# Kernel optimization log

Hardware: AMD Instinct MI355X
Metric: run time of the kernel (lower is better)

The kernel has to match this reference:

```python
import jax, jax.numpy as jnp
import numpy as np

NUM_HEADS = 12


def setup_inputs() -> dict:
    key = jax.random.key(0)
    k1, k2, k3 = jax.random.split(key, 3)
    B, N, C = 64, 320, 768
    x = jax.random.normal(k1, (B, N, C), dtype=jnp.float32)
    W_qkv = jax.random.normal(k2, (C, 3 * C), dtype=jnp.float32) * (C ** -0.5)
    W_proj = jax.random.normal(k3, (C, C), dtype=jnp.float32) * (C ** -0.5)
    b_proj = jnp.zeros((C,), dtype=jnp.float32)
    return {"x": x, "W_qkv": W_qkv, "W_proj": W_proj, "b_proj": b_proj,
            "t_h": 8, "t_w": 8, "s_h": 16, "s_w": 16}


def reference(x, W_qkv, W_proj, b_proj, t_h, t_w, s_h, s_w):
    B, N, C = x.shape
    H = NUM_HEADS
    Dh = C // H
    scale = Dh ** -0.5
    L = t_h * t_w  # template length; search length = s_h*s_w = N - L

    qkv = (x @ W_qkv).reshape(B, N, 3, H, Dh)
    q = jnp.transpose(qkv[:, :, 0], (0, 2, 1, 3))  # [B,H,N,Dh]
    k = jnp.transpose(qkv[:, :, 1], (0, 2, 1, 3))
    v = jnp.transpose(qkv[:, :, 2], (0, 2, 1, 3))

    q_mt, q_s = q[:, :, :L], q[:, :, L:]
    k_mt = k[:, :, :L]
    v_mt = v[:, :, :L]

    # Template self-attention (template attends only to template)
    attn_mt = jax.nn.softmax(jnp.einsum('bhqd,bhkd->bhqk', q_mt * scale, k_mt), axis=-1)
    x_mt = jnp.einsum('bhqk,bhkd->bhqd', attn_mt, v_mt)  # [B,H,L,Dh]

    # Search cross-attention (search attends to all tokens)
    attn_s = jax.nn.softmax(jnp.einsum('bhqd,bhkd->bhqk', q_s * scale, k), axis=-1)
    x_s = jnp.einsum('bhqk,bhkd->bhqd', attn_s, v)  # [B,H,N-L,Dh]

    x_mt = jnp.transpose(x_mt, (0, 2, 1, 3)).reshape(B, L, C)
    x_s = jnp.transpose(x_s, (0, 2, 1, 3)).reshape(B, N - L, C)
    out = jnp.concatenate([x_mt, x_s], axis=1)  # [B,N,C]
    out = out @ W_proj + b_proj
    return out
```

## Files before the change

kernel.cpp:

```cpp
#include <hip/hip_runtime.h>
#include <hip/hip_bf16.h>
#include <stdint.h>

#define BB 64
#define NN 320
#define CC 768
#define HH 12
#define DH 64
#define NC3 2304
#define MROWS (BB*NN)

typedef __attribute__((ext_vector_type(8))) short short8;
typedef __attribute__((ext_vector_type(4))) float f32x4;
typedef __attribute__((ext_vector_type(8))) __bf16 bf16x8;

union BF8U { short8 s; bf16x8 b; };
static __device__ __forceinline__ bf16x8 asbf(short8 v){ BF8U u; u.s = v; return u.b; }

#define MFMA16(a,b,c) __builtin_amdgcn_mfma_f32_16x16x32_bf16((a),(b),(c),0,0,0)

static __device__ __forceinline__ void gload16(const void* g, void* l){
  __builtin_amdgcn_global_load_lds(
      (const __attribute__((address_space(1))) void*)g,
      (__attribute__((address_space(3))) void*)l, 16, 0, 0);
}

__global__ __launch_bounds__(256) void convert_wT(
    const float* __restrict__ in, __hip_bfloat16* __restrict__ outT,
    int K, int Nc)
{
  __shared__ __hip_bfloat16 t[64][72];
  const int n0 = blockIdx.x * 64, k0 = blockIdx.y * 64;
  const int tid = threadIdx.x;
  const int tx = tid & 15, ty = tid >> 4;

  #pragma unroll
  for (int i = 0; i < 4; ++i){
    int kl = ty + i * 16;
    float4 v = *reinterpret_cast<const float4*>(&in[(size_t)(k0 + kl) * Nc + n0 + tx * 4]);
    t[tx*4+0][kl] = __float2bfloat16(v.x);
    t[tx*4+1][kl] = __float2bfloat16(v.y);
    t[tx*4+2][kl] = __float2bfloat16(v.z);
    t[tx*4+3][kl] = __float2bfloat16(v.w);
  }
  __syncthreads();
  #pragma unroll
  for (int j = 0; j < 2; ++j){
    int nl = (tid >> 3) + j * 32;
    int kl = (tid & 7) * 8;
    short8 v = *reinterpret_cast<const short8*>(&t[nl][kl]);
    *reinterpret_cast<short8*>(&outT[(size_t)(n0 + nl) * K + k0 + kl]) = v;
  }
}

__global__ __launch_bounds__(256) void convert_x(
    const float* __restrict__ X, __hip_bfloat16* __restrict__ Xb)
{
  size_t i = ((size_t)blockIdx.x * 256 + threadIdx.x) * 8;
  float4 a = *reinterpret_cast<const float4*>(&X[i]);
  float4 b = *reinterpret_cast<const float4*>(&X[i + 4]);
  __hip_bfloat16 t[8] = {__float2bfloat16(a.x), __float2bfloat16(a.y),
                         __float2bfloat16(a.z), __float2bfloat16(a.w),
                         __float2bfloat16(b.x), __float2bfloat16(b.y),
                         __float2bfloat16(b.z), __float2bfloat16(b.w)};
  *reinterpret_cast<short8*>(&Xb[i]) = *reinterpret_cast<const short8*>(t);
}

#define BM 128
#define BN 128
#define BK 64
#define NT (CC/BK)

__global__ __launch_bounds__(256, 4) void gemm_qkv(
    const __hip_bfloat16* __restrict__ Xb,
    const __hip_bfloat16* __restrict__ WT,
    __hip_bfloat16* __restrict__ qb,
    __hip_bfloat16* __restrict__ kb,
    __hip_bfloat16* __restrict__ vt)
{
  __shared__ __hip_bfloat16 As[BM][BK];
  __shared__ __hip_bfloat16 Bs[BN][BK];
  const int tid = threadIdx.x;
  const int bm = blockIdx.x * BM;
  const int bn = blockIdx.y * BN;
  const int w = tid >> 6, lane = tid & 63;
  const int wr = w >> 1, wc = w & 1;
  const int l16 = lane & 15, lq = lane >> 4;
  const int srow = lane >> 3;
  const int scol = ((lane & 7) ^ srow) * 8;
  const int rsw  = (l16 & 7) * 8;

  f32x4 acc[4][4];
  #pragma unroll
  for (int i = 0; i < 4; ++i)
    #pragma unroll
    for (int j = 0; j < 4; ++j) acc[i][j] = (f32x4){0.f,0.f,0.f,0.f};

  for (int k0 = 0; k0 < CC; k0 += BK){
    #pragma unroll
    for (int it = 0; it < 4; ++it){
      int c = w * 4 + it;
      int row = c * 8 + srow;
      gload16(&Xb[(size_t)(bm + row) * CC + k0 + scol], &As[0][0] + c * 512);
      gload16(&WT[(size_t)(bn + row) * CC + k0 + scol], &Bs[0][0] + c * 512);
    }
    __syncthreads();
    #pragma unroll
    for (int kc = 0; kc < 2; ++kc){
      const int acol = (kc*32 + lq*8) ^ rsw;
      short8 bfr[4];
      #pragma unroll
      for (int ni = 0; ni < 4; ++ni)
        bfr[ni] = *reinterpret_cast<const short8*>(&Bs[wc*64 + ni*16 + l16][acol]);
      #pragma unroll
      for (int mi = 0; mi < 4; ++mi){
        short8 af = *reinterpret_cast<const short8*>(&As[wr*64 + mi*16 + l16][acol]);
        #pragma unroll
        for (int ni = 0; ni < 4; ++ni)
          acc[mi][ni] = MFMA16(asbf(af), asbf(bfr[ni]), acc[mi][ni]);
      }
    }
    __syncthreads();
  }

  #pragma unroll
  for (int mi = 0; mi < 4; ++mi){
    #pragma unroll
    for (int ni = 0; ni < 4; ++ni){
      #pragma unroll
      for (int r = 0; r < 4; ++r){
        int row = bm + wr*64 + mi*16 + lq*4 + r;
        int col = bn + wc*64 + ni*16 + l16;
        float val = acc[mi][ni][r];
        int b = row / NN, n = row % NN;
        int s = col / CC, rem = col % CC;
        int h = rem >> 6, dh = rem & 63;
        int bh = b * HH + h;
        __hip_bfloat16 bv = __float2bfloat16(val);
        if (s == 0)      qb[((size_t)bh * NN + n) * DH + dh] = bv;
        else if (s == 1) kb[((size_t)bh * NN + n) * DH + dh] = bv;
        else             vt[((size_t)bh * DH + dh) * NN + n] = bv;
      }
    }
  }
}

template<int NKT>
__global__ __launch_bounds__(256) void attn_kernel(
    const __hip_bfloat16* __restrict__ qb,
    const __hip_bfloat16* __restrict__ kb,
    const __hip_bfloat16* __restrict__ vt,
    __hip_bfloat16* __restrict__ ob)
{
  constexpr int NTILE = NKT / 4;
  constexpr int NBUF  = (NTILE > 1) ? 2 : 1;
  __shared__ __hip_bfloat16 Kt[NBUF][64][64];
  __shared__ __hip_bfloat16 Vt[NBUF][64][64];
  __shared__ __hip_bfloat16 P[4][16][72];

  const int tid = threadIdx.x;
  const int w = tid >> 6, lane = tid & 63;
  const int l16 = lane & 15, lq = lane >> 4;
  const int srow = lane >> 3;
  const int scol = ((lane & 7) ^ srow) * 8;
  const int rsw  = (l16 & 7) * 8;

  int bh, qbase;
  if (NKT == 4){ bh = blockIdx.x;      qbase = 0; }
  else         { bh = blockIdx.x >> 2; qbase = 64 + (blockIdx.x & 3) * 64; }
  const int qrow0 = qbase + w * 16;

  const __hip_bfloat16* qp = qb + ((size_t)bh * NN + qrow0) * DH;
  const __hip_bfloat16* kp = kb + (size_t)bh * NN * DH;
  const __hip_bfloat16* vp = vt + (size_t)bh * DH * NN;

  short8 aq[2];
  #pragma unroll
  for (int kc = 0; kc < 2; ++kc)
    aq[kc] = *reinterpret_cast<const short8*>(&qp[l16 * DH + kc*32 + lq*8]);
  __builtin_amdgcn_sched_barrier(0);

  auto stageK = [&](int j){
    #pragma unroll
    for (int it = 0; it < 2; ++it){
      int c = w * 2 + it;
      gload16(&kp[(size_t)(j*64 + c*8 + srow) * DH + scol],
              &Kt[j & (NBUF-1)][0][0] + c * 512);
    }
  };
  auto stageV = [&](int j){
    #pragma unroll
    for (int it = 0; it < 2; ++it){
      int c = w * 2 + it;
      gload16(&vp[(size_t)(c*8 + srow) * NN + j*64 + scol],
              &Vt[j & (NBUF-1)][0][0] + c * 512);
    }
  };

  f32x4 s[NKT];
  #pragma unroll
  for (int kt = 0; kt < NKT; ++kt) s[kt] = (f32x4){0.f,0.f,0.f,0.f};

  stageK(0);
  if (NTILE > 1) stageK(1);
  #pragma unroll
  for (int j = 0; j < NTILE; ++j){
    if (j + 1 < NTILE) asm volatile("s_waitcnt vmcnt(2)" ::: "memory");
    else               asm volatile("s_waitcnt vmcnt(0)" ::: "memory");
    __builtin_amdgcn_s_barrier();
    #pragma unroll
    for (int kc = 0; kc < 2; ++kc){
      const int acol = (kc*32 + lq*8) ^ rsw;
      #pragma unroll
      for (int ktl = 0; ktl < 4; ++ktl){
        short8 bk = *reinterpret_cast<const short8*>(&Kt[j & (NBUF-1)][ktl*16 + l16][acol]);
        s[j*4 + ktl] = MFMA16(asbf(aq[kc]), asbf(bk), s[j*4 + ktl]);
      }
    }
    __builtin_amdgcn_s_barrier();
    if (j + 2 < NTILE) stageK(j + 2);
  }

  stageV(0);
  if (NTILE > 1) stageV(1);

  const float scale = 0.125f;
  float sum[4];
  #pragma unroll
  for (int r = 0; r < 4; ++r){
    float mx = -1e30f;
    #pragma unroll
    for (int kt = 0; kt < NKT; ++kt) mx = fmaxf(mx, s[kt][r]);
    #pragma unroll
    for (int off = 1; off < 16; off <<= 1) mx = fmaxf(mx, __shfl_xor(mx, off));
    float sm = 0.f;
    #pragma unroll
    for (int kt = 0; kt < NKT; ++kt){
      float p = __expf((s[kt][r] - mx) * scale);
      __hip_bfloat16 pb = __float2bfloat16(p);
      s[kt][r] = __bfloat162float(pb);
      sm += __bfloat162float(pb);
    }
    #pragma unroll
    for (int off = 1; off < 16; off <<= 1) sm += __shfl_xor(sm, off);
    sum[r] = sm;
  }

  f32x4 o[4];
  #pragma unroll
  for (int nt = 0; nt < 4; ++nt) o[nt] = (f32x4){0.f,0.f,0.f,0.f};
  #pragma unroll
  for (int j = 0; j < NTILE; ++j){
    if (j + 1 < NTILE) asm volatile("s_waitcnt vmcnt(2)" ::: "memory");
    else               asm volatile("s_waitcnt vmcnt(0)" ::: "memory");
    __builtin_amdgcn_s_barrier();
    #pragma unroll
    for (int ktl = 0; ktl < 4; ++ktl)
      #pragma unroll
      for (int r = 0; r < 4; ++r)
        P[w][lq*4 + r][ktl*16 + l16] = __float2bfloat16(s[j*4 + ktl][r]);
    #pragma unroll
    for (int kc = 0; kc < 2; ++kc){
      short8 ap = *reinterpret_cast<const short8*>(&P[w][l16][kc*32 + lq*8]);
      const int vcol = (kc*32 + lq*8) ^ rsw;
      #pragma unroll
      for (int nt = 0; nt < 4; ++nt){
        short8 bv = *reinterpret_cast<const short8*>(&Vt[j & (NBUF-1)][nt*16 + l16][vcol]);
        o[nt] = MFMA16(asbf(ap), asbf(bv), o[nt]);
      }
    }
    __builtin_amdgcn_s_barrier();
    if (j + 2 < NTILE) stageV(j + 2);
  }

  const int b = bh / HH, h = bh % HH;
  #pragma unroll
  for (int nt = 0; nt < 4; ++nt){
    #pragma unroll
    for (int r = 0; r < 4; ++r){
      int qrow = qrow0 + lq*4 + r;
      int dh = nt*16 + l16;
      float val = o[nt][r] / sum[r];
      ob[((size_t)b * NN + qrow) * CC + h * DH + dh] = __float2bfloat16(val);
    }
  }
}

__global__ __launch_bounds__(256, 4) void gemm_proj(
    const __hip_bfloat16* __restrict__ A,
    const __hip_bfloat16* __restrict__ WT,
    const float* __restrict__ bias,
    float* __restrict__ out)
{
  __shared__ __hip_bfloat16 As[BM][BK];
  __shared__ __hip_bfloat16 Bs[BN][BK];
  const int tid = threadIdx.x;
  const int bm = blockIdx.x * BM;
  const int bn = blockIdx.y * BN;
  const int w = tid >> 6, lane = tid & 63;
  const int wr = w >> 1, wc = w & 1;
  const int l16 = lane & 15, lq = lane >> 4;
  const int srow = lane >> 3;
  const int scol = ((lane & 7) ^ srow) * 8;
  const int rsw  = (l16 & 7) * 8;

  f32x4 acc[4][4];
  #pragma unroll
  for (int i = 0; i < 4; ++i)
    #pragma unroll
    for (int j = 0; j < 4; ++j) acc[i][j] = (f32x4){0.f,0.f,0.f,0.f};

  for (int k0 = 0; k0 < CC; k0 += BK){
    #pragma unroll
    for (int it = 0; it < 4; ++it){
      int c = w * 4 + it;
      int row = c * 8 + srow;
      gload16(&A [(size_t)(bm + row) * CC + k0 + scol], &As[0][0] + c * 512);
      gload16(&WT[(size_t)(bn + row) * CC + k0 + scol], &Bs[0][0] + c * 512);
    }
    __syncthreads();
    #pragma unroll
    for (int kc = 0; kc < 2; ++kc){
      const int acol = (kc*32 + lq*8) ^ rsw;
      short8 bfr[4];
      #pragma unroll
      for (int ni = 0; ni < 4; ++ni)
        bfr[ni] = *reinterpret_cast<const short8*>(&Bs[wc*64 + ni*16 + l16][acol]);
      #pragma unroll
      for (int mi = 0; mi < 4; ++mi){
        short8 af = *reinterpret_cast<const short8*>(&As[wr*64 + mi*16 + l16][acol]);
        #pragma unroll
        for (int ni = 0; ni < 4; ++ni)
          acc[mi][ni] = MFMA16(asbf(af), asbf(bfr[ni]), acc[mi][ni]);
      }
    }
    __syncthreads();
  }

  #pragma unroll
  for (int mi = 0; mi < 4; ++mi){
    #pragma unroll
    for (int ni = 0; ni < 4; ++ni){
      #pragma unroll
      for (int r = 0; r < 4; ++r){
        int row = bm + wr*64 + mi*16 + lq*4 + r;
        int col = bn + wc*64 + ni*16 + l16;
        out[(size_t)row * CC + col] = acc[mi][ni][r] + bias[col];
      }
    }
  }
}

extern "C" void kernel_launch(void* const* d_in, const int* in_sizes, int n_in,
                              void* d_out, int out_size, void* d_ws, size_t ws_size,
                              hipStream_t stream)
{
  const float* x     = (const float*)d_in[0];
  const float* Wqkv  = (const float*)d_in[1];
  const float* Wproj = (const float*)d_in[2];
  const float* bproj = (const float*)d_in[3];
  float* out = (float*)d_out;

  char* ws = (char*)d_ws;
  __hip_bfloat16* wqkvT  = (__hip_bfloat16*)ws; ws += (size_t)NC3 * CC * 2;
  __hip_bfloat16* wprojT = (__hip_bfloat16*)ws; ws += (size_t)CC * CC * 2;
  __hip_bfloat16* xb     = (__hip_bfloat16*)ws; ws += (size_t)MROWS * CC * 2;
  const size_t headsz = (size_t)BB * HH * NN * DH * 2;
  __hip_bfloat16* qb = (__hip_bfloat16*)ws; ws += headsz;
  __hip_bfloat16* kb = (__hip_bfloat16*)ws; ws += headsz;
  __hip_bfloat16* vt = (__hip_bfloat16*)ws; ws += headsz;
  __hip_bfloat16* ob = (__hip_bfloat16*)ws; ws += headsz;

  convert_wT<<<dim3(NC3/64, CC/64), 256, 0, stream>>>(Wqkv, wqkvT, CC, NC3);
  convert_wT<<<dim3(CC/64,  CC/64), 256, 0, stream>>>(Wproj, wprojT, CC, CC);
  convert_x<<<MROWS * CC / (256*8), 256, 0, stream>>>(x, xb);
  gemm_qkv<<<dim3(MROWS / BM, NC3 / BN), 256, 0, stream>>>(xb, wqkvT, qb, kb, vt);
  attn_kernel<4><<<BB * HH, 256, 0, stream>>>(qb, kb, vt, ob);
  attn_kernel<20><<<BB * HH * 4, 256, 0, stream>>>(qb, kb, vt, ob);
  gemm_proj<<<dim3(MROWS / BM, CC / BN), 256, 0, stream>>>(ob, wprojT, bproj, out);
}
```

Before: 228.0 us.

## Enlarge GEMM tiles to 256x256 with double-buffered async LDS loads

Both GEMMs move from 128x128 tiles on 256 threads to 256x256 tiles on 512 threads (8 waves, each computing 128x64). LDS is double-buffered so the next K-tile's global-to-LDS loads are issued before computing the current one, with vmcnt waits replacing the full syncs. MFMA groups are wrapped in setprio to favour the matrix pipe. This aims to raise data reuse and hide load latency, but leaves fewer blocks for the small proj GEMM (240 blocks) and uses 128KB of dynamic LDS per block.

```diff
diff --git a/kernel.cpp b/kernel.cpp
--- a/kernel.cpp
+++ b/kernel.cpp
@@ -66,70 +66,98 @@
   *reinterpret_cast<short8*>(&Xb[i]) = *reinterpret_cast<const short8*>(t);
 }
 
-#define BM 128
-#define BN 128
+#define BM 256
+#define BN 256
 #define BK 64
 #define NT (CC/BK)
-
-__global__ __launch_bounds__(256, 4) void gemm_qkv(
+#define GBUF 32768
+
+__global__ __launch_bounds__(512, 2) void gemm_qkv(
     const __hip_bfloat16* __restrict__ Xb,
     const __hip_bfloat16* __restrict__ WT,
     __hip_bfloat16* __restrict__ qb,
     __hip_bfloat16* __restrict__ kb,
     __hip_bfloat16* __restrict__ vt)
 {
-  __shared__ __hip_bfloat16 As[BM][BK];
-  __shared__ __hip_bfloat16 Bs[BN][BK];
+  extern __shared__ __hip_bfloat16 lds[];
   const int tid = threadIdx.x;
   const int bm = blockIdx.x * BM;
   const int bn = blockIdx.y * BN;
   const int w = tid >> 6, lane = tid & 63;
-  const int wr = w >> 1, wc = w & 1;
+  const int wr = w >> 2, wc = w & 3;
   const int l16 = lane & 15, lq = lane >> 4;
   const int srow = lane >> 3;
   const int scol = ((lane & 7) ^ srow) * 8;
   const int rsw  = (l16 & 7) * 8;
-
-  f32x4 acc[4][4];
-  #pragma unroll
-  for (int i = 0; i < 4; ++i)
+  const int chunk = w * 4;
+
+  f32x4 acc[8][4];
+  #pragma unroll
+  for (int i = 0; i < 8; ++i)
     #pragma unroll
     for (int j = 0; j < 4; ++j) acc[i][j] = (f32x4){0.f,0.f,0.f,0.f};
 
-  for (int k0 = 0; k0 < CC; k0 += BK){
+  auto stage = [&](int t){
+    __hip_bfloat16* as = lds + (t & 1) * GBUF;
+    __hip_bfloat16* bs = as + 16384;
+    const int k0 = t * BK;
     #pragma unroll
     for (int it = 0; it < 4; ++it){
-      int c = w * 4 + it;
+      int c = chunk + it;
       int row = c * 8 + srow;
-      gload16(&Xb[(size_t)(bm + row) * CC + k0 + scol], &As[0][0] + c * 512);
-      gload16(&WT[(size_t)(bn + row) * CC + k0 + scol], &Bs[0][0] + c * 512);
-    }
-    __syncthreads();
+      gload16(&Xb[(size_t)(bm + row) * CC + k0 + scol], as + c * 512);
+      gload16(&WT[(size_t)(bn + row) * CC + k0 + scol], bs + c * 512);
+    }
+  };
+
+  stage(0);
+  #pragma unroll 2
+  for (int t = 0; t < NT; ++t){
+    if (t + 1 < NT){
+      stage(t + 1);
+      __builtin_amdgcn_sched_barrier(0);
+      asm volatile("s_waitcnt vmcnt(8)" ::: "memory");
+    } else {
+      asm volatile("s_waitcnt vmcnt(0)" ::: "memory");
+    }
+    __builtin_amdgcn_s_barrier();
+    const __hip_bfloat16* as = lds + (t & 1) * GBUF;
+    const __hip_bfloat16* bs = as + 16384;
     #pragma unroll
     for (int kc = 0; kc < 2; ++kc){
       const int acol = (kc*32 + lq*8) ^ rsw;
-      short8 bfr[4];
+      short8 bfr[4], af[8];
       #pragma unroll
       for (int ni = 0; ni < 4; ++ni)
-        bfr[ni] = *reinterpret_cast<const short8*>(&Bs[wc*64 + ni*16 + l16][acol]);
-      #pragma unroll
-      for (int mi = 0; mi < 4; ++mi){
-        short8 af = *reinterpret_cast<const short8*>(&As[wr*64 + mi*16 + l16][acol]);
+        bfr[ni] = *reinterpret_cast<const short8*>(bs + (wc*64 + ni*16 + l16) * BK + acol);
+      #pragma unroll
+      for (int mi = 0; mi < 8; ++mi)
+        af[mi] = *reinterpret_cast<const short8*>(as + (wr*128 + mi*16 + l16) * BK + acol);
+      __builtin_amdgcn_s_setprio(1);
+      #pragma unroll
+      for (int mi = 0; mi < 4; ++mi)
         #pragma unroll
         for (int ni = 0; ni < 4; ++ni)
-          acc[mi][ni] = MFMA16(asbf(af), asbf(bfr[ni]), acc[mi][ni]);
-      }
-    }
-    __syncthreads();
-  }
-
-  #pragma unroll
-  for (int mi = 0; mi < 4; ++mi){
+          acc[mi][ni] = MFMA16(asbf(af[mi]), asbf(bfr[ni]), acc[mi][ni]);
+      __builtin_amdgcn_s_setprio(0);
+      __builtin_amdgcn_s_setprio(1);
+      #pragma unroll
+      for (int mi = 4; mi < 8; ++mi)
+        #pragma unroll
+        for (int ni = 0; ni < 4; ++ni)
+          acc[mi][ni] = MFMA16(asbf(af[mi]), asbf(bfr[ni]), acc[mi][ni]);
+      __builtin_amdgcn_s_setprio(0);
+    }
+    __builtin_amdgcn_s_barrier();
+  }
+
+  #pragma unroll
+  for (int mi = 0; mi < 8; ++mi){
     #pragma unroll
     for (int ni = 0; ni < 4; ++ni){
       #pragma unroll
       for (int r = 0; r < 4; ++r){
-        int row = bm + wr*64 + mi*16 + lq*4 + r;
+        int row = bm + wr*128 + mi*16 + lq*4 + r;
         int col = bn + wc*64 + ni*16 + l16;
         float val = acc[mi][ni][r];
         int b = row / NN, n = row % NN;
@@ -286,64 +314,91 @@
   }
 }
 
-__global__ __launch_bounds__(256, 4) void gemm_proj(
+__global__ __launch_bounds__(512, 2) void gemm_proj(
     const __hip_bfloat16* __restrict__ A,
     const __hip_bfloat16* __restrict__ WT,
     const float* __restrict__ bias,
     float* __restrict__ out)
 {
-  __shared__ __hip_bfloat16 As[BM][BK];
-  __shared__ __hip_bfloat16 Bs[BN][BK];
+  extern __shared__ __hip_bfloat16 lds[];
   const int tid = threadIdx.x;
   const int bm = blockIdx.x * BM;
   const int bn = blockIdx.y * BN;
   const int w = tid >> 6, lane = tid & 63;
-  const int wr = w >> 1, wc = w & 1;
+  const int wr = w >> 2, wc = w & 3;
   const int l16 = lane & 15, lq = lane >> 4;
   const int srow = lane >> 3;
   const int scol = ((lane & 7) ^ srow) * 8;
   const int rsw  = (l16 & 7) * 8;
-
-  f32x4 acc[4][4];
-  #pragma unroll
-  for (int i = 0; i < 4; ++i)
+  const int chunk = w * 4;
+
+  f32x4 acc[8][4];
+  #pragma unroll
+  for (int i = 0; i < 8; ++i)
     #pragma unroll
     for (int j = 0; j < 4; ++j) acc[i][j] = (f32x4){0.f,0.f,0.f,0.f};
 
-  for (int k0 = 0; k0 < CC; k0 += BK){
+  auto stage = [&](int t){
+    __hip_bfloat16* as = lds + (t & 1) * GBUF;
+    __hip_bfloat16* bs = as + 16384;
+    const int k0 = t * BK;
     #pragma unroll
     for (int it = 0; it < 4; ++it){
-      int c = w * 4 + it;
+      int c = chunk + it;
       int row = c * 8 + srow;
-      gload16(&A [(size_t)(bm + row) * CC + k0 + scol], &As[0][0] + c * 512);
-      gload16(&WT[(size_t)(bn + row) * CC + k0 + scol], &Bs[0][0] + c * 512);
-    }
-    __syncthreads();
+      gload16(&A [(size_t)(bm + row) * CC + k0 + scol], as + c * 512);
+      gload16(&WT[(size_t)(bn + row) * CC + k0 + scol], bs + c * 512);
+    }
+  };
+
+  stage(0);
+  #pragma unroll 2
+  for (int t = 0; t < NT; ++t){
+    if (t + 1 < NT){
+      stage(t + 1);
+      __builtin_amdgcn_sched_barrier(0);
+      asm volatile("s_waitcnt vmcnt(8)" ::: "memory");
+    } else {
+      asm volatile("s_waitcnt vmcnt(0)" ::: "memory");
+    }
+    __builtin_amdgcn_s_barrier();
+    const __hip_bfloat16* as = lds + (t & 1) * GBUF;
+    const __hip_bfloat16* bs = as + 16384;
     #pragma unroll
     for (int kc = 0; kc < 2; ++kc){
       const int acol = (kc*32 + lq*8) ^ rsw;
-      short8 bfr[4];
+      short8 bfr[4], af[8];
       #pragma unroll
       for (int ni = 0; ni < 4; ++ni)
-        bfr[ni] = *reinterpret_cast<const short8*>(&Bs[wc*64 + ni*16 + l16][acol]);
-      #pragma unroll
-      for (int mi = 0; mi < 4; ++mi){
-        short8 af = *reinterpret_cast<const short8*>(&As[wr*64 + mi*16 + l16][acol]);
+        bfr[ni] = *reinterpret_cast<const short8*>(bs + (wc*64 + ni*16 + l16) * BK + acol);
+      #pragma unroll
+      for (int mi = 0; mi < 8; ++mi)
+        af[mi] = *reinterpret_cast<const short8*>(as + (wr*128 + mi*16 + l16) * BK + acol);
+      __builtin_amdgcn_s_setprio(1);
+      #pragma unroll
+      for (int mi = 0; mi < 4; ++mi)
         #pragma unroll
         for (int ni = 0; ni < 4; ++ni)
-          acc[mi][ni] = MFMA16(asbf(af), asbf(bfr[ni]), acc[mi][ni]);
-      }
-    }
-    __syncthreads();
-  }
-
-  #pragma unroll
-  for (int mi = 0; mi < 4; ++mi){
+          acc[mi][ni] = MFMA16(asbf(af[mi]), asbf(bfr[ni]), acc[mi][ni]);
+      __builtin_amdgcn_s_setprio(0);
+      __builtin_amdgcn_s_setprio(1);
+      #pragma unroll
+      for (int mi = 4; mi < 8; ++mi)
+        #pragma unroll
+        for (int ni = 0; ni < 4; ++ni)
+          acc[mi][ni] = MFMA16(asbf(af[mi]), asbf(bfr[ni]), acc[mi][ni]);
+      __builtin_amdgcn_s_setprio(0);
+    }
+    __builtin_amdgcn_s_barrier();
+  }
+
+  #pragma unroll
+  for (int mi = 0; mi < 8; ++mi){
     #pragma unroll
     for (int ni = 0; ni < 4; ++ni){
       #pragma unroll
       for (int r = 0; r < 4; ++r){
-        int row = bm + wr*64 + mi*16 + lq*4 + r;
+        int row = bm + wr*128 + mi*16 + lq*4 + r;
         int col = bn + wc*64 + ni*16 + l16;
         out[(size_t)row * CC + col] = acc[mi][ni][r] + bias[col];
       }
@@ -371,11 +426,13 @@
   __hip_bfloat16* vt = (__hip_bfloat16*)ws; ws += headsz;
   __hip_bfloat16* ob = (__hip_bfloat16*)ws; ws += headsz;
 
+  const size_t ldsbytes = 2 * (size_t)GBUF * sizeof(__hip_bfloat16);
+
   convert_wT<<<dim3(NC3/64, CC/64), 256, 0, stream>>>(Wqkv, wqkvT, CC, NC3);
   convert_wT<<<dim3(CC/64,  CC/64), 256, 0, stream>>>(Wproj, wprojT, CC, CC);
   convert_x<<<MROWS * CC / (256*8), 256, 0, stream>>>(x, xb);
-  gemm_qkv<<<dim3(MROWS / BM, NC3 / BN), 256, 0, stream>>>(xb, wqkvT, qb, kb, vt);
+  gemm_qkv<<<dim3(MROWS / BM, NC3 / BN), 512, ldsbytes, stream>>>(xb, wqkvT, qb, kb, vt);
   attn_kernel<4><<<BB * HH, 256, 0, stream>>>(qb, kb, vt, ob);
   attn_kernel<20><<<BB * HH * 4, 256, 0, stream>>>(qb, kb, vt, ob);
-  gemm_proj<<<dim3(MROWS / BM, CC / BN), 256, 0, stream>>>(ob, wprojT, bproj, out);
-}
+  gemm_proj<<<dim3(MROWS / BM, CC / BN), 512, ldsbytes, stream>>>(ob, wprojT, bproj, out);
+}
```

After: 310.4 us. 36.1% more time.
